# Optimization experiments

Measured on AMD Instinct MI355X. Metric: run time of the kernel, lower is better.

## Reference

```python
import jax, jax.numpy as jnp
import numpy as np

KS = 5          # dilated_kernel_size
LIM = KS // 2   # positions live in [-2, 2]
B = 2048


def _construct_kernel(w, p1, p2):
    """DCLS v1ste kernel construction.
    w, p1, p2: (Cout, Cin, kernel_count) -> dense kernel (Cout, Cin, KS, KS).
    Forward: each element's weight is scattered to the NEAREST integer grid
    position (straight-through rounding of the bilinear fractional parts).
    """
    q1 = p1 + LIM
    q2 = p2 + LIM
    i1 = jnp.floor(q1)
    i2 = jnp.floor(q2)
    r1 = q1 - i1
    r2 = q2 - i2
    # straight-through estimator: forward = hard round, backward = identity
    r1 = jax.lax.stop_gradient(jnp.where(r1 >= 0.5, 1.0, 0.0) - r1) + r1
    r2 = jax.lax.stop_gradient(jnp.where(r2 >= 0.5, 1.0, 0.0) - r2) + r2
    i1 = i1.astype(jnp.int32)
    i2 = i2.astype(jnp.int32)
    # one_hot of out-of-range index is all-zero, which drops invalid neighbors
    a = (1.0 - r1)[..., None] * jax.nn.one_hot(i1, KS) + r1[..., None] * jax.nn.one_hot(i1 + 1, KS)
    b = (1.0 - r2)[..., None] * jax.nn.one_hot(i2, KS) + r2[..., None] * jax.nn.one_hot(i2 + 1, KS)
    return jnp.einsum('oik,oika,oikb->oiab', w, a, b)


def _conv(x, k, pad):
    return jax.lax.conv_general_dilated(x, k, (1, 1), [(pad, pad), (pad, pad)])


def _maxpool2(x):
    return jax.lax.reduce_window(x, -jnp.inf, jax.lax.max, (1, 1, 2, 2), (1, 1, 2, 2), 'VALID')


def setup_inputs() -> dict:
    key = jax.random.key(0)
    ks = jax.random.split(key, 12)
    x = jax.random.normal(ks[0], (B, 1, 28, 28), dtype=jnp.float32)
    w1 = jax.random.normal(ks[1], (32, 1, 26), dtype=jnp.float32) * 0.2
    p1 = jax.random.uniform(ks[2], (32, 1, 26), minval=-LIM, maxval=LIM, dtype=jnp.float32)
    p2 = jax.random.uniform(ks[3], (32, 1, 26), minval=-LIM, maxval=LIM, dtype=jnp.float32)
    b1 = jnp.zeros((32,), dtype=jnp.float32)
    w2 = jax.random.normal(ks[4], (64, 32, 3, 3), dtype=jnp.float32) * 0.06
    b2 = jnp.zeros((64,), dtype=jnp.float32)
    fc1_w = jax.random.normal(ks[5], (128, 64 * 14 * 14), dtype=jnp.float32) * 0.009
    fc1_b = jnp.zeros((128,), dtype=jnp.float32)
    fc2_w = jax.random.normal(ks[6], (10, 128), dtype=jnp.float32) * 0.09
    fc2_b = jnp.zeros((10,), dtype=jnp.float32)
    return {"x": x, "w1": w1, "p1": p1, "p2": p2, "b1": b1, "w2": w2,
            "b2": b2, "fc1_w": fc1_w, "fc1_b": fc1_b, "fc2_w": fc2_w, "fc2_b": fc2_b}


def reference(x, w1, p1, p2, b1, w2, b2, fc1_w, fc1_b, fc2_w, fc2_b):
    k1 = _construct_kernel(w1, p1, p2)                      # (32,1,5,5)
    h = jax.nn.relu(_conv(x, k1, 2) + b1[None, :, None, None])   # (B,32,28,28)
    h = jax.nn.relu(_conv(h, w2, 1) + b2[None, :, None, None])   # (B,64,28,28)
    h = _maxpool2(h)                                        # (B,64,14,14)
    h = h.reshape(-1, 64 * 14 * 14)
    h = jax.nn.relu(h @ fc1_w.T + fc1_b)
    return h @ fc2_w.T + fc2_b
```

## Files before the change

### kernel.cpp

```cpp
#include <hip/hip_runtime.h>
#include <hip/hip_bf16.h>

typedef __attribute__((ext_vector_type(8))) short bf16x8;
typedef __attribute__((ext_vector_type(4))) float f32x4;
typedef __attribute__((ext_vector_type(4))) unsigned int u32x4;
typedef __attribute__((ext_vector_type(2))) unsigned int u32x2;

#define NB 2048

static __device__ __forceinline__ unsigned short f2bf(float f) {
  unsigned int u = __builtin_bit_cast(unsigned int, f);
  u += 0x7fffu + ((u >> 16) & 1u);
  return (unsigned short)(u >> 16);
}
static __device__ __forceinline__ unsigned int cvtpk(float lo, float hi) {
  unsigned int r;
  asm("v_cvt_pk_bf16_f32 %0, %1, %2" : "=v"(r) : "v"(lo), "v"(hi));
  return r;
}

__global__ __launch_bounds__(256) void k_prep(
    const float* __restrict__ w2, const float* __restrict__ fc1w,
    const float* __restrict__ w1, const float* __restrict__ p1,
    const float* __restrict__ p2,
    unsigned short* __restrict__ w2b, unsigned short* __restrict__ fc1wb,
    unsigned short* __restrict__ k1b) {
  const int gid = blockIdx.x * blockDim.x + threadIdx.x;
  if (gid < 401408) {
    const int j0 = gid * 4;
    const int kw = j0 & 31;
    const int n  = (j0 >> 5) & 127;
    const int q  = j0 >> 12;
    f32x4 v = *(const f32x4*)&fc1w[n*12544 + q*32 + kw];
    u32x2 r = { cvtpk(v[0], v[1]), cvtpk(v[2], v[3]) };
    *(u32x2*)&fc1wb[j0] = r;
  } else if (gid < 401408 + 18432) {
    int i = gid - 401408;
    int cin = i & 31;
    int cout = (i >> 5) & 63;
    int kk = i >> 11;
    int ky = kk / 3, kx = kk % 3;
    w2b[i] = f2bf(w2[((cout*32 + cin)*3 + ky)*3 + kx]);
  } else if (gid < 401408 + 18432 + 1024) {
    int t = gid - (401408 + 18432);
    int o = t >> 5, tap = t & 31;
    unsigned short r = 0;
    if (tap < 25) {
      int a = tap / 5, bcol = tap % 5;
      float acc = 0.f;
      for (int k = 0; k < 26; ++k) {
        float q1 = p1[o*26 + k] + 2.0f;
        float q2 = p2[o*26 + k] + 2.0f;
        float f1 = floorf(q1), f2 = floorf(q2);
        int idx1 = (int)f1 + ((q1 - f1) >= 0.5f ? 1 : 0);
        int idx2 = (int)f2 + ((q2 - f2) >= 0.5f ? 1 : 0);
        if (idx1 == a && idx2 == bcol) acc += w1[o*26 + k];
      }
      r = f2bf(acc);
    }
    k1b[t] = r;
  }
}

__global__ __launch_bounds__(256, 3) void k_conv(
    const float* __restrict__ x, const unsigned short* __restrict__ k1b,
    const float* __restrict__ b1, const unsigned short* __restrict__ w2b,
    const float* __restrict__ b2, unsigned short* __restrict__ h3) {
  __shared__ __align__(16) float xs[32*36];
  __shared__ __align__(16) unsigned short h1s[16*32*32];

  const int t = threadIdx.x;
  const int bimg = (blockIdx.x & 7) * 256 + (blockIdx.x >> 3);
  const int lane = t & 63;
  const int wid = t >> 6;
  const int l15 = lane & 15;
  const int lk = lane >> 4;

  for (int i = t; i < 1152; i += 256) {
    int iy = i / 36, ix = i - iy*36;
    float v = 0.f;
    if (iy >= 2 && iy < 30 && ix >= 2 && ix < 30)
      v = x[bimg*784 + (iy-2)*28 + (ix-2)];
    xs[i] = v;
  }

  int off[8];
  #pragma unroll
  for (int j = 0; j < 8; ++j) {
    int tp = lk*8 + j; tp = tp > 24 ? 24 : tp;
    int ky = tp / 5;
    off[j] = ky*36 + (tp - ky*5);
  }
  const bf16x8 k1a0 = *(const bf16x8*)&k1b[l15*32 + lk*8];
  const bf16x8 k1a1 = *(const bf16x8*)&k1b[(16 + l15)*32 + lk*8];
  f32x4 b1i0, b1i1;
  #pragma unroll
  for (int r = 0; r < 4; ++r) {
    b1i0[r] = b1[lk*4 + r];
    b1i1[r] = b1[16 + lk*4 + r];
  }

  const int ntp = wid & 1;
  const int tx  = wid >> 1;
  bf16x8 bfr[2][9];
  #pragma unroll
  for (int nn = 0; nn < 2; ++nn)
    #pragma unroll
    for (int kk = 0; kk < 9; ++kk)
      bfr[nn][kk] = *(const bf16x8*)&w2b[(kk*64 + (ntp*2+nn)*16 + l15)*32 + lk*8];
  f32x4 b2i[2];
  #pragma unroll
  for (int nn = 0; nn < 2; ++nn) {
    float bb = b2[ntp*32 + nn*16 + l15];
    b2i[nn] = (f32x4){bb, bb, bb, bb};
  }
  int colOff[3];
  #pragma unroll
  for (int kx = 0; kx < 3; ++kx) {
    int xk = tx*16 + l15 + kx; xk = xk > 31 ? 31 : xk;
    colOff[kx] = xk*64 + ((lk ^ ((xk >> 1) & 3)) << 4);
  }

  const int mtile = bimg >> 4, mi = bimg & 15;
  unsigned short* h3m = h3 + (size_t)mtile*200704 + mi*32;

  __syncthreads();

  for (int half = 0; half < 2; ++half) {
    if (half) __syncthreads();

    {
      u32x4* H = (u32x4*)h1s;
      u32x4 z = {0u,0u,0u,0u};
      const int zrow = half ? 15 : 0;
      if (t < 128) H[zrow*128 + t] = z;
      const int r0 = half ? 0 : 1;
      if (t < 240) {
        int rr = t >> 4, rem = t & 15;
        int pi = rem >> 2, sub = rem & 3;
        int px = pi == 0 ? 0 : 28 + pi;
        H[((r0 + rr)*32 + px)*4 + sub] = z;
      }
    }

    const int ybase = half ? 13 : 0;
    for (int tid = wid; tid < 30; tid += 4) {
      const int ty = tid >> 1;
      const int x0 = (tid & 1) << 4;
      const int yo = ybase + ty;
      const float* bp = &xs[yo*36 + x0 + l15];
      u32x4 bw;
      bw[0] = cvtpk(bp[off[0]], bp[off[1]]);
      bw[1] = cvtpk(bp[off[2]], bp[off[3]]);
      bw[2] = cvtpk(bp[off[4]], bp[off[5]]);
      bw[3] = cvtpk(bp[off[6]], bp[off[7]]);
      const bf16x8 bfrag = __builtin_bit_cast(bf16x8, bw);
      f32x4 d0 = b1i0, d1 = b1i1;
      d0 = __builtin_amdgcn_mfma_f32_16x16x32_bf16(k1a0, bfrag, d0, 0, 0, 0);
      d1 = __builtin_amdgcn_mfma_f32_16x16x32_bf16(k1a1, bfrag, d1, 0, 0, 0);
      const int xo = x0 + l15;
      if (xo < 28) {
        const int ry = half ? (yo - 13) : (yo + 1);
        const int pix = ry*32 + xo + 1;
        const int swz = (pix >> 1) & 3;
        const int blkbase = (lk >> 1);
        unsigned int w0lo = cvtpk(fmaxf(d0[0], 0.f), fmaxf(d0[1], 0.f));
        unsigned int w0hi = cvtpk(fmaxf(d0[2], 0.f), fmaxf(d0[3], 0.f));
        unsigned int w1lo = cvtpk(fmaxf(d1[0], 0.f), fmaxf(d1[1], 0.f));
        unsigned int w1hi = cvtpk(fmaxf(d1[2], 0.f), fmaxf(d1[3], 0.f));
        char* base = (char*)h1s + pix*64 + (lk & 1)*8;
        *(u32x2*)(base + ((blkbase ^ swz) << 4))       = (u32x2){w0lo, w0hi};
        *(u32x2*)(base + (((2 + blkbase) ^ swz) << 4)) = (u32x2){w1lo, w1hi};
      }
    }
    __syncthreads();

    const char* h1c = (const char*)h1s;
    for (int pyl = 0; pyl < 7; ++pyl) {
      const int py = half*7 + pyl;
      const int rbase = pyl*2*2048;
      f32x4 acc[2][2];
      #pragma unroll
      for (int yi = 0; yi < 2; ++yi)
        #pragma unroll
        for (int nn = 0; nn < 2; ++nn) acc[yi][nn] = b2i[nn];
      #pragma unroll
      for (int kx = 0; kx < 3; ++kx) {
        bf16x8 af[4];
        #pragma unroll
        for (int r = 0; r < 4; ++r)
          af[r] = *(const bf16x8*)(h1c + rbase + r*2048 + colOff[kx]);
        #pragma unroll
        for (int ky = 0; ky < 3; ++ky)
          #pragma unroll
          for (int yi = 0; yi < 2; ++yi) {
            acc[yi][0] = __builtin_amdgcn_mfma_f32_16x16x32_bf16(af[yi+ky], bfr[0][ky*3+kx], acc[yi][0], 0, 0, 0);
            acc[yi][1] = __builtin_amdgcn_mfma_f32_16x16x32_bf16(af[yi+ky], bfr[1][ky*3+kx], acc[yi][1], 0, 0, 0);
          }
      }
      if (!(tx == 1 && lk == 3)) {
        const int px0 = tx*8 + lk*2;
        #pragma unroll
        for (int nn = 0; nn < 2; ++nn) {
          float q0 = fmaxf(fmaxf(fmaxf(acc[0][nn][0], acc[0][nn][1]),
                                 fmaxf(acc[1][nn][0], acc[1][nn][1])), 0.f);
          float q1 = fmaxf(fmaxf(fmaxf(acc[0][nn][2], acc[0][nn][3]),
                                 fmaxf(acc[1][nn][2], acc[1][nn][3])), 0.f);
          const int c = ntp*32 + nn*16 + l15;
          const int k0 = c*196 + py*14 + px0;
          *(unsigned int*)&h3m[(k0 >> 5)*512 + (k0 & 31)] = cvtpk(q0, q1);
        }
      }
    }
  }
}

__global__ __launch_bounds__(512) void k_fc1(const unsigned short* __restrict__ h3,
                                             const unsigned short* __restrict__ fc1wb,
                                             float* __restrict__ h4p) {
  const int bid = blockIdx.x;
  const int m4 = bid >> 3, kh = bid & 7;
  const int t = threadIdx.x, lane = t & 63, w = t >> 6;
  const int rg = w >> 2;
  const int nw = w & 3;
  const int l15 = lane & 15, lk = lane >> 4;
  const int lo = l15*32 + lk*8;

  const unsigned short* a0p = h3 + (size_t)(m4*4 + rg*2)*200704 + (size_t)(kh*49)*512 + lo;
  const unsigned short* a1p = a0p + 200704;
  const unsigned short* b0p = fc1wb + (size_t)(kh*49)*4096 + (nw*32)*32 + lo;

  f32x4 acc00 = {0.f,0.f,0.f,0.f}, acc01 = {0.f,0.f,0.f,0.f};
  f32x4 acc10 = {0.f,0.f,0.f,0.f}, acc11 = {0.f,0.f,0.f,0.f};
  #pragma unroll
  for (int ks = 0; ks < 49; ++ks) {
    bf16x8 a0 = *(const bf16x8*)(a0p + ks*512);
    bf16x8 a1 = *(const bf16x8*)(a1p + ks*512);
    bf16x8 w0 = *(const bf16x8*)(b0p + ks*4096);
    bf16x8 w1 = *(const bf16x8*)(b0p + ks*4096 + 512);
    acc00 = __builtin_amdgcn_mfma_f32_16x16x32_bf16(a0, w0, acc00, 0, 0, 0);
    acc01 = __builtin_amdgcn_mfma_f32_16x16x32_bf16(a0, w1, acc01, 0, 0, 0);
    acc10 = __builtin_amdgcn_mfma_f32_16x16x32_bf16(a1, w0, acc10, 0, 0, 0);
    acc11 = __builtin_amdgcn_mfma_f32_16x16x32_bf16(a1, w1, acc11, 0, 0, 0);
  }
  float* outp = h4p + (size_t)kh * NB * 128;
  const int n0 = nw*32 + l15;
  const int bb0 = m4*64 + rg*32 + lk*4;
  #pragma unroll
  for (int jj = 0; jj < 4; ++jj) {
    outp[(bb0 + jj)*128 + n0]           = acc00[jj];
    outp[(bb0 + jj)*128 + n0 + 16]      = acc01[jj];
    outp[(bb0 + 16 + jj)*128 + n0]      = acc10[jj];
    outp[(bb0 + 16 + jj)*128 + n0 + 16] = acc11[jj];
  }
}

__global__ __launch_bounds__(256) void k_fc2(const float* __restrict__ h4p,
                                             const float* __restrict__ fc1b,
                                             const float* __restrict__ fc2w,
                                             const float* __restrict__ fc2b,
                                             float* __restrict__ out) {
  __shared__ float hs[8*129];
  const int blk = blockIdx.x;
  const int t = threadIdx.x;
  for (int i = t; i < 1024; i += 256) {
    const int base = blk*1024 + i;
    float v = 0.f;
    #pragma unroll
    for (int kh = 0; kh < 8; ++kh) v += h4p[base + kh*262144];
    v += fc1b[i & 127];
    hs[(i >> 7)*129 + (i & 127)] = fmaxf(v, 0.f);
  }
  __syncthreads();
  if (t < 80) {
    const int bb = t / 10, n = t - (t/10)*10;
    float acc = fc2b[n];
    const float* wr = fc2w + n*128;
    const float* hr = hs + bb*129;
    #pragma unroll 8
    for (int k = 0; k < 128; ++k) acc = fmaf(hr[k], wr[k], acc);
    out[(blk*8 + bb)*10 + n] = acc;
  }
}

extern "C" void kernel_launch(void* const* d_in, const int* in_sizes, int n_in,
                              void* d_out, int out_size, void* d_ws, size_t ws_size,
                              hipStream_t stream) {
  const float* x    = (const float*)d_in[0];
  const float* w1   = (const float*)d_in[1];
  const float* p1   = (const float*)d_in[2];
  const float* p2   = (const float*)d_in[3];
  const float* b1   = (const float*)d_in[4];
  const float* w2   = (const float*)d_in[5];
  const float* b2   = (const float*)d_in[6];
  const float* fc1w = (const float*)d_in[7];
  const float* fc1b = (const float*)d_in[8];
  const float* fc2w = (const float*)d_in[9];
  const float* fc2b = (const float*)d_in[10];

  if (ws_size < 63021056u) return;
  char* ws = (char*)d_ws;
  unsigned short* k1b  = (unsigned short*)(ws + 0);
  unsigned short* w2b  = (unsigned short*)(ws + 4096);
  unsigned short* fc1wb= (unsigned short*)(ws + 40960);
  unsigned short* h3   = (unsigned short*)(ws + 3252224);
  float* h4p           = (float*)(ws + 54632448);

  k_prep<<<(401408 + 18432 + 1024 + 255) / 256, 256, 0, stream>>>(
      w2, fc1w, w1, p1, p2, w2b, fc1wb, k1b);
  k_conv<<<NB, 256, 0, stream>>>(x, k1b, b1, w2b, b2, h3);
  k_fc1<<<256, 512, 0, stream>>>(h3, fc1wb, h4p);
  k_fc2<<<256, 256, 0, stream>>>(h4p, fc1b, fc2w, fc2b, (float*)d_out);
}
```

Baseline: 106.1 us.

## Fuse fc2 into fc1 via last-block split-K reduction with atomic counters

Removes the separate fc2 kernel. Each fc1 block now writes its split-K partial tile contiguously and increments a per-row-group atomic counter. The last of the 8 K-slice blocks sums the partials, applies bias and ReLU, then computes fc2 from shared memory. This saves a kernel launch and gives the partial writes a coalesced layout, at the cost of threadfences, an atomic, and serialized tail work in the last block. The block index mapping is also swapped so the K-slices of the same row group are spread apart in launch order.

```diff
diff --git a/kernel.cpp b/kernel.cpp
--- a/kernel.cpp
+++ b/kernel.cpp
@@ -24,7 +24,7 @@
     const float* __restrict__ w1, const float* __restrict__ p1,
     const float* __restrict__ p2,
     unsigned short* __restrict__ w2b, unsigned short* __restrict__ fc1wb,
-    unsigned short* __restrict__ k1b) {
+    unsigned short* __restrict__ k1b, int* __restrict__ cnt) {
   const int gid = blockIdx.x * blockDim.x + threadIdx.x;
   if (gid < 401408) {
     const int j0 = gid * 4;
@@ -59,6 +59,8 @@
       r = f2bf(acc);
     }
     k1b[t] = r;
+  } else if (gid < 401408 + 18432 + 1024 + 32) {
+    cnt[gid - (401408 + 18432 + 1024)] = 0;
   }
 }
 
@@ -217,9 +219,16 @@
 
 __global__ __launch_bounds__(512) void k_fc1(const unsigned short* __restrict__ h3,
                                              const unsigned short* __restrict__ fc1wb,
-                                             float* __restrict__ h4p) {
+                                             const float* __restrict__ fc1b,
+                                             const float* __restrict__ fc2w,
+                                             const float* __restrict__ fc2b,
+                                             float* __restrict__ h4p,
+                                             int* __restrict__ cnt,
+                                             float* __restrict__ out) {
+  __shared__ float hs[64*132];
+  __shared__ int lastflag;
   const int bid = blockIdx.x;
-  const int m4 = bid >> 3, kh = bid & 7;
+  const int kh = bid >> 5, m4 = bid & 31;
   const int t = threadIdx.x, lane = t & 63, w = t >> 6;
   const int rg = w >> 2;
   const int nw = w & 3;
@@ -243,43 +252,48 @@
     acc10 = __builtin_amdgcn_mfma_f32_16x16x32_bf16(a1, w0, acc10, 0, 0, 0);
     acc11 = __builtin_amdgcn_mfma_f32_16x16x32_bf16(a1, w1, acc11, 0, 0, 0);
   }
-  float* outp = h4p + (size_t)kh * NB * 128;
-  const int n0 = nw*32 + l15;
-  const int bb0 = m4*64 + rg*32 + lk*4;
-  #pragma unroll
-  for (int jj = 0; jj < 4; ++jj) {
-    outp[(bb0 + jj)*128 + n0]           = acc00[jj];
-    outp[(bb0 + jj)*128 + n0 + 16]      = acc01[jj];
-    outp[(bb0 + 16 + jj)*128 + n0]      = acc10[jj];
-    outp[(bb0 + 16 + jj)*128 + n0 + 16] = acc11[jj];
-  }
-}
-
-__global__ __launch_bounds__(256) void k_fc2(const float* __restrict__ h4p,
-                                             const float* __restrict__ fc1b,
-                                             const float* __restrict__ fc2w,
-                                             const float* __restrict__ fc2b,
-                                             float* __restrict__ out) {
-  __shared__ float hs[8*129];
-  const int blk = blockIdx.x;
-  const int t = threadIdx.x;
-  for (int i = t; i < 1024; i += 256) {
-    const int base = blk*1024 + i;
-    float v = 0.f;
+  {
+    float* op = h4p + (size_t)bid*8192 + t*16;
+    *(f32x4*)(op + 0)  = acc00;
+    *(f32x4*)(op + 4)  = acc01;
+    *(f32x4*)(op + 8)  = acc10;
+    *(f32x4*)(op + 12) = acc11;
+  }
+  __threadfence();
+  if (t == 0) lastflag = atomicAdd(&cnt[m4], 1);
+  __syncthreads();
+  if (lastflag != 7) return;
+  __threadfence();
+
+  f32x4 v[4] = {{0.f,0.f,0.f,0.f},{0.f,0.f,0.f,0.f},{0.f,0.f,0.f,0.f},{0.f,0.f,0.f,0.f}};
+  for (int k2 = 0; k2 < 8; ++k2) {
+    const float* ip = h4p + (size_t)(k2*32 + m4)*8192 + t*16;
     #pragma unroll
-    for (int kh = 0; kh < 8; ++kh) v += h4p[base + kh*262144];
-    v += fc1b[i & 127];
-    hs[(i >> 7)*129 + (i & 127)] = fmaxf(v, 0.f);
-  }
+    for (int r4 = 0; r4 < 4; ++r4) {
+      f32x4 u = *(const f32x4*)(ip + r4*4);
+      v[r4][0] += u[0]; v[r4][1] += u[1]; v[r4][2] += u[2]; v[r4][3] += u[3];
+    }
+  }
+  #pragma unroll
+  for (int pairhi = 0; pairhi < 2; ++pairhi)
+    #pragma unroll
+    for (int pairlo = 0; pairlo < 2; ++pairlo)
+      #pragma unroll
+      for (int jj = 0; jj < 4; ++jj) {
+        const int r = (pairhi*2 + pairlo)*4 + jj;
+        const int bb = rg*32 + pairhi*16 + lk*4 + jj;
+        const int n  = nw*32 + pairlo*16 + l15;
+        hs[bb*132 + n] = fmaxf(v[r >> 2][r & 3] + fc1b[n], 0.f);
+      }
   __syncthreads();
-  if (t < 80) {
-    const int bb = t / 10, n = t - (t/10)*10;
-    float acc = fc2b[n];
-    const float* wr = fc2w + n*128;
-    const float* hr = hs + bb*129;
+  for (int j = t; j < 640; j += 512) {
+    const int bb = j / 10, n2 = j - (j/10)*10;
+    float acc = fc2b[n2];
+    const float* wr = fc2w + n2*128;
+    const float* hr = hs + bb*132;
     #pragma unroll 8
     for (int k = 0; k < 128; ++k) acc = fmaf(hr[k], wr[k], acc);
-    out[(blk*8 + bb)*10 + n] = acc;
+    out[(m4*64 + bb)*10 + n2] = acc;
   }
 }
 
@@ -298,17 +312,17 @@
   const float* fc2w = (const float*)d_in[9];
   const float* fc2b = (const float*)d_in[10];
 
-  if (ws_size < 63021056u) return;
+  if (ws_size < 63021184u) return;
   char* ws = (char*)d_ws;
   unsigned short* k1b  = (unsigned short*)(ws + 0);
   unsigned short* w2b  = (unsigned short*)(ws + 4096);
   unsigned short* fc1wb= (unsigned short*)(ws + 40960);
   unsigned short* h3   = (unsigned short*)(ws + 3252224);
   float* h4p           = (float*)(ws + 54632448);
-
-  k_prep<<<(401408 + 18432 + 1024 + 255) / 256, 256, 0, stream>>>(
-      w2, fc1w, w1, p1, p2, w2b, fc1wb, k1b);
+  int* cnt             = (int*)(ws + 63021056);
+
+  k_prep<<<(401408 + 18432 + 1024 + 32 + 255) / 256, 256, 0, stream>>>(
+      w2, fc1w, w1, p1, p2, w2b, fc1wb, k1b, cnt);
   k_conv<<<NB, 256, 0, stream>>>(x, k1b, b1, w2b, b2, h3);
-  k_fc1<<<256, 512, 0, stream>>>(h3, fc1wb, h4p);
-  k_fc2<<<256, 256, 0, stream>>>(h4p, fc1b, fc2w, fc2b, (float*)d_out);
-}
+  k_fc1<<<256, 512, 0, stream>>>(h3, fc1wb, fc1b, fc2w, fc2b, h4p, cnt, (float*)d_out);
+}
```

New measurement: 191.4 us. +80.4%, slower.
